# Kernel optimization log

Measured on AMD Instinct MI355X. Metric: run time of the kernel, lower is better.

## Reference

```python
import jax, jax.numpy as jnp
import numpy as np

NUM_NODES = 100000
NUM_EDGES = 3200000
D_IN, D_HID, D_OUT = 64, 64, 32


def setup_inputs() -> dict:
    key = jax.random.key(0)
    k1, k2, k3, k4, k5 = jax.random.split(key, 5)
    edge_index = jax.random.randint(k1, (2, NUM_EDGES), 0, NUM_NODES, dtype=jnp.int64)
    edge_weight = jax.random.uniform(k2, (NUM_EDGES,), dtype=jnp.float32)
    emb = jax.random.normal(k3, (NUM_NODES, D_IN), dtype=jnp.float32)
    # glorot-ish scaled weights for the two GCNConv layers
    W1 = jax.random.normal(k4, (D_IN, D_HID), dtype=jnp.float32) * (1.0 / np.sqrt(D_IN))
    b1 = jnp.zeros((D_HID,), dtype=jnp.float32)
    W2 = jax.random.normal(k5, (D_HID, D_OUT), dtype=jnp.float32) * (1.0 / np.sqrt(D_HID))
    b2 = jnp.zeros((D_OUT,), dtype=jnp.float32)
    return {"edge_index": edge_index, "edge_weight": edge_weight,
            "emb": emb, "W1": W1, "b1": b1, "W2": W2, "b2": b2}


def reference(edge_index, edge_weight, emb, W1, b1, W2, b2):
    N = emb.shape[0]
    row, col = edge_index[0], edge_index[1]
    # PyG gcn_norm: add self-loops (weight 1.0), symmetric normalization
    loop = jnp.arange(N, dtype=edge_index.dtype)
    row_f = jnp.concatenate([row, loop])
    col_f = jnp.concatenate([col, loop])
    ew_f = jnp.concatenate([edge_weight, jnp.ones((N,), dtype=edge_weight.dtype)])
    deg = jax.ops.segment_sum(ew_f, col_f, num_segments=N)          # [N]
    deg_inv_sqrt = jnp.where(deg > 0, jax.lax.rsqrt(deg), 0.0)      # inf -> 0
    norm = deg_inv_sqrt[row_f] * ew_f * deg_inv_sqrt[col_f]         # [E+N]

    def gcn_conv(x, W, b):
        x = x @ W                                                    # [N, d_out]
        msg = x[row_f] * norm[:, None]                               # [E+N, d_out]
        out = jax.ops.segment_sum(msg, col_f, num_segments=N)       # [N, d_out]
        return out + b

    x = jax.nn.relu(gcn_conv(emb, W1, b1))
    x = gcn_conv(x, W2, b2)
    # F.normalize(p=2, dim=1, eps=1e-12)
    l2 = jnp.linalg.norm(x, axis=1, keepdims=True)
    return x / jnp.maximum(l2, 1e-12)
```

## Files before the change

### kernel.cpp

```cpp
#include <hip/hip_runtime.h>
#include <hip/hip_fp16.h>
#include <math.h>

#define THREADS 256
#define BWIDTH 512
#define BSHIFT 9
#define CHUNK 3125

__global__ void init_kernel(const int* __restrict__ ei32, int* __restrict__ flag,
                            unsigned int* __restrict__ gcnt) {
    int t = threadIdx.x;
    gcnt[t] = 0u;
    if (t == 0) {
        int z = (ei32[1] == 0) + (ei32[3] == 0) + (ei32[5] == 0) + (ei32[7] == 0);
        *flag = (z == 4) ? 1 : 0;
    }
}

__device__ __forceinline__ int edge_at(const void* ei, int is64, size_t idx) {
    return is64 ? (int)((const long long*)ei)[idx] : ((const int*)ei)[idx];
}

__global__ void p1_count_kernel(const void* __restrict__ ei, const int* __restrict__ flag,
                                unsigned int* __restrict__ gcnt, unsigned int* __restrict__ table,
                                int E, int B) {
    __shared__ unsigned int lcnt[256];
    int t = threadIdx.x, b = blockIdx.x;
    lcnt[t] = 0u;
    __syncthreads();
    int is64 = *flag;
    int base = b * CHUNK;
    int end = min(E, base + CHUNK);
    for (int e = base + t; e < end; e += THREADS) {
        int c = edge_at(ei, is64, (size_t)E + e);
        atomicAdd(&lcnt[c >> BSHIFT], 1u);
    }
    __syncthreads();
    if (t < B) table[(size_t)b * 256 + t] = atomicAdd(&gcnt[t], lcnt[t]);
}

__global__ void p2_scan_kernel(const unsigned int* __restrict__ gcnt,
                               unsigned int* __restrict__ bstart, int B, int E) {
    int t = threadIdx.x;
    unsigned int v = (t < B) ? gcnt[t] : 0u;
    unsigned int incl = v;
    int lane = t & 63, wid = t >> 6;
#pragma unroll
    for (int off = 1; off < 64; off <<= 1) {
        unsigned int x = __shfl_up(incl, off);
        if (lane >= off) incl += x;
    }
    __shared__ unsigned int ws4[4];
    if (lane == 63) ws4[wid] = incl;
    __syncthreads();
    unsigned int wb = 0;
    for (int w = 0; w < wid; ++w) wb += ws4[w];
    unsigned int excl = wb + incl - v;
    if (t < B) bstart[t] = excl;
    if (t == 0) bstart[B] = (unsigned int)E;
}

__global__ void p3_scatter_kernel(const void* __restrict__ ei, const float* __restrict__ ew,
                                  const int* __restrict__ flag,
                                  const unsigned int* __restrict__ bstart,
                                  const unsigned int* __restrict__ table,
                                  int2* __restrict__ out, int E, int B) {
    __shared__ int2 stage[CHUNK];
    __shared__ unsigned char lbin[CHUNK];
    __shared__ unsigned short perm[CHUNK];
    __shared__ unsigned int lcnt[256];
    __shared__ unsigned int lcur[256];
    __shared__ int shiftb[256];
    __shared__ unsigned int ws4[4];

    int t = threadIdx.x, b = blockIdx.x;
    lcnt[t] = 0u;
    __syncthreads();
    int is64 = *flag;
    int base = b * CHUNK;
    int end = min(E, base + CHUNK);
    int n = end - base;
    for (int i = t; i < n; i += THREADS) {
        int e = base + i;
        int r = edge_at(ei, is64, (size_t)e);
        int c = edge_at(ei, is64, (size_t)E + e);
        int bin = c >> BSHIFT;
        stage[i] = make_int2(r | ((c & (BWIDTH - 1)) << 17), __float_as_int(ew[e]));
        lbin[i] = (unsigned char)bin;
        atomicAdd(&lcnt[bin], 1u);
    }
    __syncthreads();
    unsigned int v = lcnt[t];
    unsigned int incl = v;
    int lane = t & 63, wid = t >> 6;
#pragma unroll
    for (int off = 1; off < 64; off <<= 1) {
        unsigned int x = __shfl_up(incl, off);
        if (lane >= off) incl += x;
    }
    if (lane == 63) ws4[wid] = incl;
    __syncthreads();
    unsigned int wb = 0;
    for (int w = 0; w < wid; ++w) wb += ws4[w];
    unsigned int excl = wb + incl - v;
    lcur[t] = excl;
    shiftb[t] = (t < B) ? ((int)(bstart[t] + table[(size_t)b * 256 + t]) - (int)excl) : 0;
    __syncthreads();
    for (int i = t; i < n; i += THREADS) {
        unsigned int pos = atomicAdd(&lcur[lbin[i]], 1u);
        perm[pos] = (unsigned short)i;
    }
    __syncthreads();
    for (int k = t; k < n; k += THREADS) {
        int i = perm[k];
        int bin = lbin[i];
        out[(size_t)(shiftb[bin] + k)] = stage[i];
    }
}

__global__ void p5_bucket_kernel(const int2* __restrict__ bucketed,
                                 const unsigned int* __restrict__ bstart,
                                 float* __restrict__ dinv, int* __restrict__ colptr,
                                 int2* __restrict__ csr, int N, int E) {
    __shared__ unsigned int cnt[BWIDTH];
    __shared__ float deg[BWIDTH];
    __shared__ unsigned int cur[BWIDTH];
    __shared__ unsigned int ws4[4];

    int t = threadIdx.x, b = blockIdx.x;
    cnt[t] = 0u; cnt[t + 256] = 0u;
    deg[t] = 0.f; deg[t + 256] = 0.f;
    __syncthreads();
    unsigned int s = bstart[b], e2 = bstart[b + 1];
    for (unsigned int j = s + t; j < e2; j += THREADS) {
        int2 v = bucketed[j];
        unsigned int cl = ((unsigned int)v.x) >> 17;
        atomicAdd(&cnt[cl], 1u);
        atomicAdd(&deg[cl], __int_as_float(v.y));
    }
    __syncthreads();
    unsigned int a0 = cnt[2 * t], a1 = cnt[2 * t + 1];
    unsigned int sum = a0 + a1;
    unsigned int incl = sum;
    int lane = t & 63, wid = t >> 6;
#pragma unroll
    for (int off = 1; off < 64; off <<= 1) {
        unsigned int x = __shfl_up(incl, off);
        if (lane >= off) incl += x;
    }
    if (lane == 63) ws4[wid] = incl;
    __syncthreads();
    unsigned int wb = 0;
    for (int w = 0; w < wid; ++w) wb += ws4[w];
    unsigned int exclT = wb + incl - sum;
    unsigned int e0 = exclT, e1 = exclT + a0;
    int node0 = b << BSHIFT;
    int n0 = node0 + 2 * t, n1 = n0 + 1;
    float d0 = rsqrtf(deg[2 * t] + 1.0f);
    float d1 = rsqrtf(deg[2 * t + 1] + 1.0f);
    if (n0 < N) { colptr[n0] = (int)(s + e0); dinv[n0] = d0; }
    if (n1 < N) { colptr[n1] = (int)(s + e1); dinv[n1] = d1; }
    deg[2 * t] = d0;
    deg[2 * t + 1] = d1;
    cur[2 * t] = s + e0;
    cur[2 * t + 1] = s + e1;
    __syncthreads();
    for (unsigned int j = s + t; j < e2; j += THREADS) {
        int2 v = bucketed[j];
        unsigned int cl = ((unsigned int)v.x) >> 17;
        unsigned int pos = atomicAdd(&cur[cl], 1u);
        float w = __int_as_float(v.y) * deg[cl];
        csr[pos] = make_int2(v.x, __float_as_int(w));
    }
    if (b == 0 && t == 0) colptr[N] = E;
}

__device__ __forceinline__ float ldf(const float* p, size_t i) { return p[i]; }
__device__ __forceinline__ float ldf(const __half* p, size_t i) { return __half2float(p[i]); }

template <typename TIN, int DOUT>
__global__ void gemm_kernel(const TIN* __restrict__ X, const float* __restrict__ W,
                            const float* __restrict__ dinv, __half* __restrict__ Y, int N) {
    constexpr int RPB = 256 / DOUT;
    __shared__ float Wl[64 * DOUT];
    __shared__ float Xl[RPB * 64];
    int tid = threadIdx.x;
    for (int i = tid; i < 64 * DOUT; i += 256) Wl[i] = W[i];
    int base = blockIdx.x * RPB;
    for (int i = tid; i < RPB * 64; i += 256) {
        int rr = base + i / 64;
        Xl[i] = (rr < N) ? ldf(X, (size_t)rr * 64 + (i & 63)) : 0.f;
    }
    __syncthreads();
    int r = tid / DOUT, c = tid % DOUT;
    int row = base + r;
    if (row < N) {
        float acc = 0.f;
#pragma unroll
        for (int k = 0; k < 64; ++k) acc = fmaf(Xl[r * 64 + k], Wl[k * DOUT + c], acc);
        Y[(size_t)row * DOUT + c] = __float2half(acc * dinv[row]);
    }
}

__global__ void agg1_kernel(const __half* __restrict__ X1, const int* __restrict__ colptr,
                            const int2* __restrict__ csr, const float* __restrict__ dinv,
                            const float* __restrict__ bias, __half* __restrict__ H, int N) {
    int tid = threadIdx.x;
    int node = blockIdx.x * 4 + (tid >> 6);
    if (node >= N) return;
    int lane = tid & 63;
    int eo = lane >> 5;
    int dp = lane & 31;
    int s = colptr[node], e = colptr[node + 1];
    float acc0 = 0.f, acc1 = 0.f;
    int j = s;
    while (j + 16 <= e) {
        int2 vv[8];
#pragma unroll
        for (int k = 0; k < 8; ++k) vv[k] = csr[j + 2 * k + eo];
        __half2 hh[8];
#pragma unroll
        for (int k = 0; k < 8; ++k) {
            int r = vv[k].x & 0x1FFFF;
            hh[k] = *(const __half2*)(X1 + ((size_t)r << 6) + (dp << 1));
        }
#pragma unroll
        for (int k = 0; k < 8; ++k) {
            float2 x = __half22float2(hh[k]);
            float w = __int_as_float(vv[k].y);
            acc0 = fmaf(w, x.x, acc0);
            acc1 = fmaf(w, x.y, acc1);
        }
        j += 16;
    }
    for (; j < e; j += 2) {
        int jj = j + eo;
        float w = 0.f;
        int r = 0;
        if (jj < e) { int2 v = csr[jj]; r = v.x & 0x1FFFF; w = __int_as_float(v.y); }
        __half2 h = *(const __half2*)(X1 + ((size_t)r << 6) + (dp << 1));
        float2 x = __half22float2(h);
        acc0 = fmaf(w, x.x, acc0);
        acc1 = fmaf(w, x.y, acc1);
    }
    acc0 += __shfl_xor(acc0, 32);
    acc1 += __shfl_xor(acc1, 32);
    if (eo == 0) {
        float di = dinv[node];
        __half2 hs = *(const __half2*)(X1 + ((size_t)node << 6) + (dp << 1));
        float2 xs = __half22float2(hs);
        float a0 = fmaxf(bias[2 * dp + 0] + fmaf(di, xs.x, acc0), 0.f);
        float a1 = fmaxf(bias[2 * dp + 1] + fmaf(di, xs.y, acc1), 0.f);
        *(__half2*)(H + ((size_t)node << 6) + (dp << 1)) = __floats2half2_rn(a0, a1);
    }
}

__global__ void agg2_kernel(const __half* __restrict__ X2, const int* __restrict__ colptr,
                            const int2* __restrict__ csr, const float* __restrict__ dinv,
                            const float* __restrict__ bias, float* __restrict__ out, int N) {
    int tid = threadIdx.x;
    int node = blockIdx.x * 4 + (tid >> 6);
    if (node >= N) return;
    int lane = tid & 63;
    int eo = lane >> 4;
    int dp = lane & 15;
    int s = colptr[node], e = colptr[node + 1];
    float acc0 = 0.f, acc1 = 0.f;
    int j = s;
    while (j + 16 <= e) {
        int2 vv[4];
#pragma unroll
        for (int k = 0; k < 4; ++k) vv[k] = csr[j + 4 * k + eo];
        __half2 hh[4];
#pragma unroll
        for (int k = 0; k < 4; ++k) {
            int r = vv[k].x & 0x1FFFF;
            hh[k] = *(const __half2*)(X2 + ((size_t)r << 5) + (dp << 1));
        }
#pragma unroll
        for (int k = 0; k < 4; ++k) {
            float2 x = __half22float2(hh[k]);
            float w = __int_as_float(vv[k].y);
            acc0 = fmaf(w, x.x, acc0);
            acc1 = fmaf(w, x.y, acc1);
        }
        j += 16;
    }
    for (; j < e; j += 4) {
        int jj = j + eo;
        float w = 0.f;
        int r = 0;
        if (jj < e) { int2 v = csr[jj]; r = v.x & 0x1FFFF; w = __int_as_float(v.y); }
        __half2 h = *(const __half2*)(X2 + ((size_t)r << 5) + (dp << 1));
        float2 x = __half22float2(h);
        acc0 = fmaf(w, x.x, acc0);
        acc1 = fmaf(w, x.y, acc1);
    }
    acc0 += __shfl_xor(acc0, 16);
    acc1 += __shfl_xor(acc1, 16);
    acc0 += __shfl_xor(acc0, 32);
    acc1 += __shfl_xor(acc1, 32);
    float di = dinv[node];
    __half2 hs = *(const __half2*)(X2 + ((size_t)node << 5) + (dp << 1));
    float2 xs = __half22float2(hs);
    float a0 = bias[2 * dp + 0] + fmaf(di, xs.x, acc0);
    float a1 = bias[2 * dp + 1] + fmaf(di, xs.y, acc1);
    float ss = fmaf(a0, a0, a1 * a1);
#pragma unroll
    for (int m = 1; m <= 8; m <<= 1) ss += __shfl_xor(ss, m);
    float inv = 1.f / fmaxf(sqrtf(ss), 1e-12f);
    if (eo == 0) {
        *(float2*)(out + ((size_t)node << 5) + (dp << 1)) = make_float2(a0 * inv, a1 * inv);
    }
}

extern "C" void kernel_launch(void* const* d_in, const int* in_sizes, int n_in,
                              void* d_out, int out_size, void* d_ws, size_t ws_size,
                              hipStream_t stream) {
    const void* ei = d_in[0];
    const float* ew = (const float*)d_in[1];
    const float* emb = (const float*)d_in[2];
    const float* W1 = (const float*)d_in[3];
    const float* b1 = (const float*)d_in[4];
    const float* W2 = (const float*)d_in[5];
    const float* b2 = (const float*)d_in[6];
    float* outp = (float*)d_out;

    int E = in_sizes[0] / 2;
    int N = in_sizes[2] / 64;
    int B = (N + BWIDTH - 1) >> BSHIFT;
    int GP = (E + CHUNK - 1) / CHUNK;

    char* p = (char*)d_ws;
    auto alloc = [&](size_t bytes) {
        void* q = (void*)p;
        p += (bytes + 255) & ~(size_t)255;
        return q;
    };
    unsigned int* gcnt   = (unsigned int*)alloc(256 * 4);
    unsigned int* bstart = (unsigned int*)alloc(257 * 4);
    int*          flag   = (int*)alloc(256);
    unsigned int* table  = (unsigned int*)alloc((size_t)GP * 256 * 4);
    int2*   bucketed = (int2*)alloc((size_t)E * 8);
    int2*   csr      = (int2*)alloc(((size_t)E + 16) * 8);
    float*  dinv     = (float*)alloc((size_t)N * 4);
    int*    colptr   = (int*)alloc(((size_t)N + 1) * 4);
    __half* X1h      = (__half*)alloc((size_t)N * 64 * 2);
    __half* H        = (__half*)alloc((size_t)N * 64 * 2);
    __half* X2h      = X1h;

    init_kernel<<<1, 256, 0, stream>>>((const int*)ei, flag, gcnt);
    p1_count_kernel<<<GP, THREADS, 0, stream>>>(ei, flag, gcnt, table, E, B);
    p2_scan_kernel<<<1, 256, 0, stream>>>(gcnt, bstart, B, E);
    p3_scatter_kernel<<<GP, THREADS, 0, stream>>>(ei, ew, flag, bstart, table,
                                                  bucketed, E, B);
    p5_bucket_kernel<<<B, THREADS, 0, stream>>>(bucketed, bstart, dinv, colptr, csr, N, E);
    gemm_kernel<float, 64><<<(N + 3) / 4, THREADS, 0, stream>>>(emb, W1, dinv, X1h, N);
    agg1_kernel<<<(N + 3) / 4, THREADS, 0, stream>>>(X1h, colptr, csr, dinv, b1, H, N);
    gemm_kernel<__half, 32><<<(N + 7) / 8, THREADS, 0, stream>>>(H, W2, dinv, X2h, N);
    agg2_kernel<<<(N + 3) / 4, THREADS, 0, stream>>>(X2h, colptr, csr, dinv, b2, outp, N);
}
```

Before: 327.1 us.

## Pack CSR into 32-bit entries and aggregate feature slices in separate passes

Each CSR entry is packed into one 32-bit word holding a 17-bit source index and a 15-bit half-precision weight (sign bit dropped), halving edge-list traffic. Features are stored as 16-column slices so each aggregation pass gathers from a 3.2 MB table that fits in cache better. Aggregation runs as 4 passes for layer 1 and 2 passes for layer 2, plus a separate L2-normalize kernel. The cost is re-reading the CSR once per pass, extra launches, a temporary buffer, and lower precision on the edge weights.

```diff
diff --git a/kernel.cpp b/kernel.cpp
--- a/kernel.cpp
+++ b/kernel.cpp
@@ -19,6 +19,10 @@
 
 __device__ __forceinline__ int edge_at(const void* ei, int is64, size_t idx) {
     return is64 ? (int)((const long long*)ei)[idx] : ((const int*)ei)[idx];
+}
+
+__device__ __forceinline__ float wdec(unsigned int v) {
+    return __half2float(__ushort_as_half((unsigned short)(v & 0x7FFFu)));
 }
 
 __global__ void p1_count_kernel(const void* __restrict__ ei, const int* __restrict__ flag,
@@ -121,7 +125,7 @@
 __global__ void p5_bucket_kernel(const int2* __restrict__ bucketed,
                                  const unsigned int* __restrict__ bstart,
                                  float* __restrict__ dinv, int* __restrict__ colptr,
-                                 int2* __restrict__ csr, int N, int E) {
+                                 unsigned int* __restrict__ csrp, int N, int E) {
     __shared__ unsigned int cnt[BWIDTH];
     __shared__ float deg[BWIDTH];
     __shared__ unsigned int cur[BWIDTH];
@@ -170,148 +174,177 @@
         unsigned int cl = ((unsigned int)v.x) >> 17;
         unsigned int pos = atomicAdd(&cur[cl], 1u);
         float w = __int_as_float(v.y) * deg[cl];
-        csr[pos] = make_int2(v.x, __float_as_int(w));
+        unsigned short hb = __half_as_ushort(__float2half_rn(w));
+        csrp[pos] = (((unsigned int)v.x & 0x1FFFFu) << 15) | (unsigned int)(hb & 0x7FFFu);
     }
     if (b == 0 && t == 0) colptr[N] = E;
 }
 
-__device__ __forceinline__ float ldf(const float* p, size_t i) { return p[i]; }
-__device__ __forceinline__ float ldf(const __half* p, size_t i) { return __half2float(p[i]); }
-
-template <typename TIN, int DOUT>
-__global__ void gemm_kernel(const TIN* __restrict__ X, const float* __restrict__ W,
-                            const float* __restrict__ dinv, __half* __restrict__ Y, int N) {
-    constexpr int RPB = 256 / DOUT;
-    __shared__ float Wl[64 * DOUT];
-    __shared__ float Xl[RPB * 64];
+__global__ void gemm1_kernel(const float* __restrict__ X, const float* __restrict__ W,
+                             const float* __restrict__ dinv, __half* __restrict__ Y, int N) {
+    __shared__ float Wl[64 * 64];
+    __shared__ float Xl[4 * 64];
     int tid = threadIdx.x;
-    for (int i = tid; i < 64 * DOUT; i += 256) Wl[i] = W[i];
-    int base = blockIdx.x * RPB;
-    for (int i = tid; i < RPB * 64; i += 256) {
+    for (int i = tid; i < 64 * 64; i += 256) Wl[i] = W[i];
+    int base = blockIdx.x * 4;
+    for (int i = tid; i < 4 * 64; i += 256) {
         int rr = base + i / 64;
-        Xl[i] = (rr < N) ? ldf(X, (size_t)rr * 64 + (i & 63)) : 0.f;
-    }
-    __syncthreads();
-    int r = tid / DOUT, c = tid % DOUT;
+        Xl[i] = (rr < N) ? X[(size_t)rr * 64 + (i & 63)] : 0.f;
+    }
+    __syncthreads();
+    int r = tid >> 6, c = tid & 63;
     int row = base + r;
     if (row < N) {
         float acc = 0.f;
 #pragma unroll
-        for (int k = 0; k < 64; ++k) acc = fmaf(Xl[r * 64 + k], Wl[k * DOUT + c], acc);
-        Y[(size_t)row * DOUT + c] = __float2half(acc * dinv[row]);
-    }
-}
-
-__global__ void agg1_kernel(const __half* __restrict__ X1, const int* __restrict__ colptr,
-                            const int2* __restrict__ csr, const float* __restrict__ dinv,
-                            const float* __restrict__ bias, __half* __restrict__ H, int N) {
+        for (int k = 0; k < 64; ++k) acc = fmaf(Xl[r * 64 + k], Wl[k * 64 + c], acc);
+        Y[((size_t)(c >> 4) * N + row) * 16 + (c & 15)] = __float2half(acc * dinv[row]);
+    }
+}
+
+__global__ void gemm2_kernel(const __half* __restrict__ H, const float* __restrict__ W,
+                             const float* __restrict__ dinv, __half* __restrict__ Y, int N) {
+    __shared__ float Wl[64 * 32];
+    __shared__ float Xl[8 * 64];
+    int tid = threadIdx.x;
+    for (int i = tid; i < 64 * 32; i += 256) Wl[i] = W[i];
+    int base = blockIdx.x * 8;
+    for (int i = tid; i < 8 * 64; i += 256) {
+        int rr = base + i / 64;
+        int k = i & 63;
+        Xl[i] = (rr < N) ? __half2float(H[((size_t)(k >> 4) * N + rr) * 16 + (k & 15)]) : 0.f;
+    }
+    __syncthreads();
+    int r = tid >> 5, c = tid & 31;
+    int row = base + r;
+    if (row < N) {
+        float acc = 0.f;
+#pragma unroll
+        for (int k = 0; k < 64; ++k) acc = fmaf(Xl[r * 64 + k], Wl[k * 32 + c], acc);
+        Y[((size_t)(c >> 4) * N + row) * 16 + (c & 15)] = __float2half(acc * dinv[row]);
+    }
+}
+
+__global__ void agg1_pass_kernel(const __half* __restrict__ Xs, const int* __restrict__ colptr,
+                                 const unsigned int* __restrict__ csrp,
+                                 const float* __restrict__ dinv, const float* __restrict__ bias,
+                                 __half* __restrict__ Hs, int N) {
     int tid = threadIdx.x;
     int node = blockIdx.x * 4 + (tid >> 6);
     if (node >= N) return;
     int lane = tid & 63;
-    int eo = lane >> 5;
-    int dp = lane & 31;
+    int eo = lane >> 3;
+    int dp = lane & 7;
     int s = colptr[node], e = colptr[node + 1];
     float acc0 = 0.f, acc1 = 0.f;
     int j = s;
-    while (j + 16 <= e) {
-        int2 vv[8];
-#pragma unroll
-        for (int k = 0; k < 8; ++k) vv[k] = csr[j + 2 * k + eo];
-        __half2 hh[8];
-#pragma unroll
-        for (int k = 0; k < 8; ++k) {
-            int r = vv[k].x & 0x1FFFF;
-            hh[k] = *(const __half2*)(X1 + ((size_t)r << 6) + (dp << 1));
+    while (j + 32 <= e) {
+        unsigned int vv[4];
+#pragma unroll
+        for (int k = 0; k < 4; ++k) vv[k] = csrp[j + 8 * k + eo];
+        __half2 hh[4];
+#pragma unroll
+        for (int k = 0; k < 4; ++k) {
+            int r = (int)(vv[k] >> 15);
+            hh[k] = *(const __half2*)(Xs + ((size_t)r << 4) + (dp << 1));
         }
 #pragma unroll
-        for (int k = 0; k < 8; ++k) {
+        for (int k = 0; k < 4; ++k) {
             float2 x = __half22float2(hh[k]);
-            float w = __int_as_float(vv[k].y);
+            float w = wdec(vv[k]);
             acc0 = fmaf(w, x.x, acc0);
             acc1 = fmaf(w, x.y, acc1);
         }
-        j += 16;
-    }
-    for (; j < e; j += 2) {
+        j += 32;
+    }
+    for (; j < e; j += 8) {
         int jj = j + eo;
         float w = 0.f;
         int r = 0;
-        if (jj < e) { int2 v = csr[jj]; r = v.x & 0x1FFFF; w = __int_as_float(v.y); }
-        __half2 h = *(const __half2*)(X1 + ((size_t)r << 6) + (dp << 1));
+        if (jj < e) { unsigned int v = csrp[jj]; r = (int)(v >> 15); w = wdec(v); }
+        __half2 h = *(const __half2*)(Xs + ((size_t)r << 4) + (dp << 1));
         float2 x = __half22float2(h);
         acc0 = fmaf(w, x.x, acc0);
         acc1 = fmaf(w, x.y, acc1);
     }
-    acc0 += __shfl_xor(acc0, 32);
-    acc1 += __shfl_xor(acc1, 32);
+    acc0 += __shfl_xor(acc0, 8);  acc1 += __shfl_xor(acc1, 8);
+    acc0 += __shfl_xor(acc0, 16); acc1 += __shfl_xor(acc1, 16);
+    acc0 += __shfl_xor(acc0, 32); acc1 += __shfl_xor(acc1, 32);
     if (eo == 0) {
         float di = dinv[node];
-        __half2 hs = *(const __half2*)(X1 + ((size_t)node << 6) + (dp << 1));
+        __half2 hs = *(const __half2*)(Xs + ((size_t)node << 4) + (dp << 1));
         float2 xs = __half22float2(hs);
         float a0 = fmaxf(bias[2 * dp + 0] + fmaf(di, xs.x, acc0), 0.f);
         float a1 = fmaxf(bias[2 * dp + 1] + fmaf(di, xs.y, acc1), 0.f);
-        *(__half2*)(H + ((size_t)node << 6) + (dp << 1)) = __floats2half2_rn(a0, a1);
-    }
-}
-
-__global__ void agg2_kernel(const __half* __restrict__ X2, const int* __restrict__ colptr,
-                            const int2* __restrict__ csr, const float* __restrict__ dinv,
-                            const float* __restrict__ bias, float* __restrict__ out, int N) {
+        *(__half2*)(Hs + ((size_t)node << 4) + (dp << 1)) = __floats2half2_rn(a0, a1);
+    }
+}
+
+__global__ void agg2_pass_kernel(const __half* __restrict__ Xs, const int* __restrict__ colptr,
+                                 const unsigned int* __restrict__ csrp,
+                                 const float* __restrict__ dinv, const float* __restrict__ bias,
+                                 float* __restrict__ tempA, int ps, int N) {
     int tid = threadIdx.x;
     int node = blockIdx.x * 4 + (tid >> 6);
     if (node >= N) return;
     int lane = tid & 63;
-    int eo = lane >> 4;
-    int dp = lane & 15;
+    int eo = lane >> 3;
+    int dp = lane & 7;
     int s = colptr[node], e = colptr[node + 1];
     float acc0 = 0.f, acc1 = 0.f;
     int j = s;
-    while (j + 16 <= e) {
-        int2 vv[4];
-#pragma unroll
-        for (int k = 0; k < 4; ++k) vv[k] = csr[j + 4 * k + eo];
+    while (j + 32 <= e) {
+        unsigned int vv[4];
+#pragma unroll
+        for (int k = 0; k < 4; ++k) vv[k] = csrp[j + 8 * k + eo];
         __half2 hh[4];
 #pragma unroll
         for (int k = 0; k < 4; ++k) {
-            int r = vv[k].x & 0x1FFFF;
-            hh[k] = *(const __half2*)(X2 + ((size_t)r << 5) + (dp << 1));
+            int r = (int)(vv[k] >> 15);
+            hh[k] = *(const __half2*)(Xs + ((size_t)r << 4) + (dp << 1));
         }
 #pragma unroll
         for (int k = 0; k < 4; ++k) {
             float2 x = __half22float2(hh[k]);
-            float w = __int_as_float(vv[k].y);
+            float w = wdec(vv[k]);
             acc0 = fmaf(w, x.x, acc0);
             acc1 = fmaf(w, x.y, acc1);
         }
-        j += 16;
-    }
-    for (; j < e; j += 4) {
+        j += 32;
+    }
+    for (; j < e; j += 8) {
         int jj = j + eo;
         float w = 0.f;
         int r = 0;
-        if (jj < e) { int2 v = csr[jj]; r = v.x & 0x1FFFF; w = __int_as_float(v.y); }
-        __half2 h = *(const __half2*)(X2 + ((size_t)r << 5) + (dp << 1));
+        if (jj < e) { unsigned int v = csrp[jj]; r = (int)(v >> 15); w = wdec(v); }
+        __half2 h = *(const __half2*)(Xs + ((size_t)r << 4) + (dp << 1));
         float2 x = __half22float2(h);
         acc0 = fmaf(w, x.x, acc0);
         acc1 = fmaf(w, x.y, acc1);
     }
-    acc0 += __shfl_xor(acc0, 16);
-    acc1 += __shfl_xor(acc1, 16);
-    acc0 += __shfl_xor(acc0, 32);
-    acc1 += __shfl_xor(acc1, 32);
-    float di = dinv[node];
-    __half2 hs = *(const __half2*)(X2 + ((size_t)node << 5) + (dp << 1));
-    float2 xs = __half22float2(hs);
-    float a0 = bias[2 * dp + 0] + fmaf(di, xs.x, acc0);
-    float a1 = bias[2 * dp + 1] + fmaf(di, xs.y, acc1);
-    float ss = fmaf(a0, a0, a1 * a1);
-#pragma unroll
-    for (int m = 1; m <= 8; m <<= 1) ss += __shfl_xor(ss, m);
-    float inv = 1.f / fmaxf(sqrtf(ss), 1e-12f);
+    acc0 += __shfl_xor(acc0, 8);  acc1 += __shfl_xor(acc1, 8);
+    acc0 += __shfl_xor(acc0, 16); acc1 += __shfl_xor(acc1, 16);
+    acc0 += __shfl_xor(acc0, 32); acc1 += __shfl_xor(acc1, 32);
     if (eo == 0) {
-        *(float2*)(out + ((size_t)node << 5) + (dp << 1)) = make_float2(a0 * inv, a1 * inv);
-    }
+        float di = dinv[node];
+        __half2 hs = *(const __half2*)(Xs + ((size_t)node << 4) + (dp << 1));
+        float2 xs = __half22float2(hs);
+        float a0 = bias[2 * dp + 0] + fmaf(di, xs.x, acc0);
+        float a1 = bias[2 * dp + 1] + fmaf(di, xs.y, acc1);
+        *(float2*)(tempA + (size_t)node * 32 + ps * 16 + (dp << 1)) = make_float2(a0, a1);
+    }
+}
+
+__global__ void norm_kernel(const float* __restrict__ tempA, float* __restrict__ out, int N) {
+    int tid = threadIdx.x;
+    int node = blockIdx.x * 8 + (tid >> 5);
+    if (node >= N) return;
+    int d = tid & 31;
+    float a = tempA[(size_t)node * 32 + d];
+    float ss = a * a;
+#pragma unroll
+    for (int m = 1; m <= 16; m <<= 1) ss += __shfl_xor(ss, m);
+    out[(size_t)node * 32 + d] = a / fmaxf(sqrtf(ss), 1e-12f);
 }
 
 extern "C" void kernel_launch(void* const* d_in, const int* in_sizes, int n_in,
@@ -342,21 +375,30 @@
     int*          flag   = (int*)alloc(256);
     unsigned int* table  = (unsigned int*)alloc((size_t)GP * 256 * 4);
     int2*   bucketed = (int2*)alloc((size_t)E * 8);
-    int2*   csr      = (int2*)alloc(((size_t)E + 16) * 8);
+    unsigned int* csrp = (unsigned int*)alloc(((size_t)E + 64) * 4);
     float*  dinv     = (float*)alloc((size_t)N * 4);
     int*    colptr   = (int*)alloc(((size_t)N + 1) * 4);
     __half* X1h      = (__half*)alloc((size_t)N * 64 * 2);
     __half* H        = (__half*)alloc((size_t)N * 64 * 2);
     __half* X2h      = X1h;
+    float*  tempA    = (float*)alloc((size_t)N * 32 * 4);
 
     init_kernel<<<1, 256, 0, stream>>>((const int*)ei, flag, gcnt);
     p1_count_kernel<<<GP, THREADS, 0, stream>>>(ei, flag, gcnt, table, E, B);
     p2_scan_kernel<<<1, 256, 0, stream>>>(gcnt, bstart, B, E);
     p3_scatter_kernel<<<GP, THREADS, 0, stream>>>(ei, ew, flag, bstart, table,
                                                   bucketed, E, B);
-    p5_bucket_kernel<<<B, THREADS, 0, stream>>>(bucketed, bstart, dinv, colptr, csr, N, E);
-    gemm_kernel<float, 64><<<(N + 3) / 4, THREADS, 0, stream>>>(emb, W1, dinv, X1h, N);
-    agg1_kernel<<<(N + 3) / 4, THREADS, 0, stream>>>(X1h, colptr, csr, dinv, b1, H, N);
-    gemm_kernel<__half, 32><<<(N + 7) / 8, THREADS, 0, stream>>>(H, W2, dinv, X2h, N);
-    agg2_kernel<<<(N + 3) / 4, THREADS, 0, stream>>>(X2h, colptr, csr, dinv, b2, outp, N);
-}
+    p5_bucket_kernel<<<B, THREADS, 0, stream>>>(bucketed, bstart, dinv, colptr, csrp, N, E);
+    gemm1_kernel<<<(N + 3) / 4, THREADS, 0, stream>>>(emb, W1, dinv, X1h, N);
+    for (int s = 0; s < 4; ++s) {
+        agg1_pass_kernel<<<(N + 3) / 4, THREADS, 0, stream>>>(
+            X1h + (size_t)s * N * 16, colptr, csrp, dinv, b1 + 16 * s,
+            H + (size_t)s * N * 16, N);
+    }
+    gemm2_kernel<<<(N + 7) / 8, THREADS, 0, stream>>>(H, W2, dinv, X2h, N);
+    for (int s = 0; s < 2; ++s) {
+        agg2_pass_kernel<<<(N + 3) / 4, THREADS, 0, stream>>>(
+            X2h + (size_t)s * N * 16, colptr, csrp, dinv, b2 + 16 * s, tempA, s, N);
+    }
+    norm_kernel<<<(N + 7) / 8, THREADS, 0, stream>>>(tempA, outp, N);
+}
```

New measurement: 432.5 us. +32.2%, slower.

## Pack CSR entries into 32-bit words and use persistent GEMM kernels

Applied to the files above, without the earlier changes.

CSR entries shrink from an int2 (index plus float weight) to a single 32-bit word holding a 17-bit source index and a 15-bit fp16 weight with the sign bit dropped. Weights are nonnegative, so the sign bit is safe to drop. This halves edge-stream traffic in both aggregation passes. The aggregation loops are unrolled to 32 edges per step for more loads in flight, and the GEMMs become persistent grid-stride kernels that load W into shared memory once per block instead of once per four or eight rows. The trade-off is lower weight precision, and the index packing only works for N below 131072.

```diff
diff --git a/kernel.cpp b/kernel.cpp
--- a/kernel.cpp
+++ b/kernel.cpp
@@ -6,6 +6,8 @@
 #define BWIDTH 512
 #define BSHIFT 9
 #define CHUNK 3125
+#define G1ROWS 16
+#define G2ROWS 16
 
 __global__ void init_kernel(const int* __restrict__ ei32, int* __restrict__ flag,
                             unsigned int* __restrict__ gcnt) {
@@ -19,6 +21,10 @@
 
 __device__ __forceinline__ int edge_at(const void* ei, int is64, size_t idx) {
     return is64 ? (int)((const long long*)ei)[idx] : ((const int*)ei)[idx];
+}
+
+__device__ __forceinline__ float wdec(unsigned int v) {
+    return __half2float(__ushort_as_half((unsigned short)(v & 0x7FFFu)));
 }
 
 __global__ void p1_count_kernel(const void* __restrict__ ei, const int* __restrict__ flag,
@@ -121,7 +127,7 @@
 __global__ void p5_bucket_kernel(const int2* __restrict__ bucketed,
                                  const unsigned int* __restrict__ bstart,
                                  float* __restrict__ dinv, int* __restrict__ colptr,
-                                 int2* __restrict__ csr, int N, int E) {
+                                 unsigned int* __restrict__ csrp, int N, int E) {
     __shared__ unsigned int cnt[BWIDTH];
     __shared__ float deg[BWIDTH];
     __shared__ unsigned int cur[BWIDTH];
@@ -170,41 +176,82 @@
         unsigned int cl = ((unsigned int)v.x) >> 17;
         unsigned int pos = atomicAdd(&cur[cl], 1u);
         float w = __int_as_float(v.y) * deg[cl];
-        csr[pos] = make_int2(v.x, __float_as_int(w));
+        unsigned short hb = __half_as_ushort(__float2half_rn(w));
+        csrp[pos] = (((unsigned int)v.x & 0x1FFFFu) << 15) | (unsigned int)(hb & 0x7FFFu);
     }
     if (b == 0 && t == 0) colptr[N] = E;
 }
 
-__device__ __forceinline__ float ldf(const float* p, size_t i) { return p[i]; }
-__device__ __forceinline__ float ldf(const __half* p, size_t i) { return __half2float(p[i]); }
-
-template <typename TIN, int DOUT>
-__global__ void gemm_kernel(const TIN* __restrict__ X, const float* __restrict__ W,
-                            const float* __restrict__ dinv, __half* __restrict__ Y, int N) {
-    constexpr int RPB = 256 / DOUT;
-    __shared__ float Wl[64 * DOUT];
-    __shared__ float Xl[RPB * 64];
+__global__ void gemm1_kernel(const float* __restrict__ X, const float* __restrict__ W,
+                             const float* __restrict__ dinv, __half* __restrict__ Y,
+                             int N, int tiles) {
+    __shared__ float Wl[64 * 64];
+    __shared__ float Xl[G1ROWS * 64];
     int tid = threadIdx.x;
-    for (int i = tid; i < 64 * DOUT; i += 256) Wl[i] = W[i];
-    int base = blockIdx.x * RPB;
-    for (int i = tid; i < RPB * 64; i += 256) {
-        int rr = base + i / 64;
-        Xl[i] = (rr < N) ? ldf(X, (size_t)rr * 64 + (i & 63)) : 0.f;
-    }
-    __syncthreads();
-    int r = tid / DOUT, c = tid % DOUT;
-    int row = base + r;
-    if (row < N) {
-        float acc = 0.f;
-#pragma unroll
-        for (int k = 0; k < 64; ++k) acc = fmaf(Xl[r * 64 + k], Wl[k * DOUT + c], acc);
-        Y[(size_t)row * DOUT + c] = __float2half(acc * dinv[row]);
+    for (int i = tid; i < 64 * 64; i += 256) Wl[i] = W[i];
+    int wid = tid >> 6, c = tid & 63;
+    __syncthreads();
+    for (int tile = blockIdx.x; tile < tiles; tile += gridDim.x) {
+        int base = tile * G1ROWS;
+        for (int i = tid; i < G1ROWS * 64; i += 256) {
+            int rr = base + (i >> 6);
+            Xl[i] = (rr < N) ? X[(size_t)rr * 64 + (i & 63)] : 0.f;
+        }
+        __syncthreads();
+#pragma unroll
+        for (int rg = 0; rg < G1ROWS / 4; ++rg) {
+            int r = rg * 4 + wid;
+            int row = base + r;
+            if (row < N) {
+                float acc = 0.f;
+#pragma unroll
+                for (int k = 0; k < 64; ++k) acc = fmaf(Xl[r * 64 + k], Wl[k * 64 + c], acc);
+                Y[(size_t)row * 64 + c] = __float2half(acc * dinv[row]);
+            }
+        }
+        __syncthreads();
+    }
+}
+
+__global__ void gemm2_kernel(const __half* __restrict__ H, const float* __restrict__ W,
+                             const float* __restrict__ dinv, __half* __restrict__ Y,
+                             int N, int tiles) {
+    __shared__ float Wl[64 * 32];
+    __shared__ float Xl[G2ROWS * 64];
+    int tid = threadIdx.x;
+    for (int i = tid; i < 64 * 32; i += 256) Wl[i] = W[i];
+    int rg0 = tid >> 5, c = tid & 31;
+    __syncthreads();
+    for (int tile = blockIdx.x; tile < tiles; tile += gridDim.x) {
+        int base = tile * G2ROWS;
+        for (int i = tid; i < G2ROWS * 32; i += 256) {
+            int rr = base + (i >> 5);
+            int kk = (i & 31) << 1;
+            float2 f = make_float2(0.f, 0.f);
+            if (rr < N) f = __half22float2(*(const __half2*)(H + (size_t)rr * 64 + kk));
+            Xl[(i >> 5) * 64 + kk] = f.x;
+            Xl[(i >> 5) * 64 + kk + 1] = f.y;
+        }
+        __syncthreads();
+#pragma unroll
+        for (int rg = 0; rg < G2ROWS / 8; ++rg) {
+            int r = rg * 8 + rg0;
+            int row = base + r;
+            if (row < N) {
+                float acc = 0.f;
+#pragma unroll
+                for (int k = 0; k < 64; ++k) acc = fmaf(Xl[r * 64 + k], Wl[k * 32 + c], acc);
+                Y[(size_t)row * 32 + c] = __float2half(acc * dinv[row]);
+            }
+        }
+        __syncthreads();
     }
 }
 
 __global__ void agg1_kernel(const __half* __restrict__ X1, const int* __restrict__ colptr,
-                            const int2* __restrict__ csr, const float* __restrict__ dinv,
-                            const float* __restrict__ bias, __half* __restrict__ H, int N) {
+                            const unsigned int* __restrict__ csrp,
+                            const float* __restrict__ dinv, const float* __restrict__ bias,
+                            __half* __restrict__ H, int N) {
     int tid = threadIdx.x;
     int node = blockIdx.x * 4 + (tid >> 6);
     if (node >= N) return;
@@ -214,30 +261,30 @@
     int s = colptr[node], e = colptr[node + 1];
     float acc0 = 0.f, acc1 = 0.f;
     int j = s;
-    while (j + 16 <= e) {
-        int2 vv[8];
-#pragma unroll
-        for (int k = 0; k < 8; ++k) vv[k] = csr[j + 2 * k + eo];
-        __half2 hh[8];
-#pragma unroll
-        for (int k = 0; k < 8; ++k) {
-            int r = vv[k].x & 0x1FFFF;
+    while (j + 32 <= e) {
+        unsigned int vv[16];
+#pragma unroll
+        for (int k = 0; k < 16; ++k) vv[k] = csrp[j + 2 * k + eo];
+        __half2 hh[16];
+#pragma unroll
+        for (int k = 0; k < 16; ++k) {
+            int r = (int)(vv[k] >> 15);
             hh[k] = *(const __half2*)(X1 + ((size_t)r << 6) + (dp << 1));
         }
 #pragma unroll
-        for (int k = 0; k < 8; ++k) {
+        for (int k = 0; k < 16; ++k) {
             float2 x = __half22float2(hh[k]);
-            float w = __int_as_float(vv[k].y);
+            float w = wdec(vv[k]);
             acc0 = fmaf(w, x.x, acc0);
             acc1 = fmaf(w, x.y, acc1);
         }
-        j += 16;
+        j += 32;
     }
     for (; j < e; j += 2) {
         int jj = j + eo;
         float w = 0.f;
         int r = 0;
-        if (jj < e) { int2 v = csr[jj]; r = v.x & 0x1FFFF; w = __int_as_float(v.y); }
+        if (jj < e) { unsigned int v = csrp[jj]; r = (int)(v >> 15); w = wdec(v); }
         __half2 h = *(const __half2*)(X1 + ((size_t)r << 6) + (dp << 1));
         float2 x = __half22float2(h);
         acc0 = fmaf(w, x.x, acc0);
@@ -256,8 +303,9 @@
 }
 
 __global__ void agg2_kernel(const __half* __restrict__ X2, const int* __restrict__ colptr,
-                            const int2* __restrict__ csr, const float* __restrict__ dinv,
-                            const float* __restrict__ bias, float* __restrict__ out, int N) {
+                            const unsigned int* __restrict__ csrp,
+                            const float* __restrict__ dinv, const float* __restrict__ bias,
+                            float* __restrict__ out, int N) {
     int tid = threadIdx.x;
     int node = blockIdx.x * 4 + (tid >> 6);
     if (node >= N) return;
@@ -267,30 +315,30 @@
     int s = colptr[node], e = colptr[node + 1];
     float acc0 = 0.f, acc1 = 0.f;
     int j = s;
-    while (j + 16 <= e) {
-        int2 vv[4];
-#pragma unroll
-        for (int k = 0; k < 4; ++k) vv[k] = csr[j + 4 * k + eo];
-        __half2 hh[4];
-#pragma unroll
-        for (int k = 0; k < 4; ++k) {
-            int r = vv[k].x & 0x1FFFF;
+    while (j + 32 <= e) {
+        unsigned int vv[8];
+#pragma unroll
+        for (int k = 0; k < 8; ++k) vv[k] = csrp[j + 4 * k + eo];
+        __half2 hh[8];
+#pragma unroll
+        for (int k = 0; k < 8; ++k) {
+            int r = (int)(vv[k] >> 15);
             hh[k] = *(const __half2*)(X2 + ((size_t)r << 5) + (dp << 1));
         }
 #pragma unroll
-        for (int k = 0; k < 4; ++k) {
+        for (int k = 0; k < 8; ++k) {
             float2 x = __half22float2(hh[k]);
-            float w = __int_as_float(vv[k].y);
+            float w = wdec(vv[k]);
             acc0 = fmaf(w, x.x, acc0);
             acc1 = fmaf(w, x.y, acc1);
         }
-        j += 16;
+        j += 32;
     }
     for (; j < e; j += 4) {
         int jj = j + eo;
         float w = 0.f;
         int r = 0;
-        if (jj < e) { int2 v = csr[jj]; r = v.x & 0x1FFFF; w = __int_as_float(v.y); }
+        if (jj < e) { unsigned int v = csrp[jj]; r = (int)(v >> 15); w = wdec(v); }
         __half2 h = *(const __half2*)(X2 + ((size_t)r << 5) + (dp << 1));
         float2 x = __half22float2(h);
         acc0 = fmaf(w, x.x, acc0);
@@ -342,21 +390,24 @@
     int*          flag   = (int*)alloc(256);
     unsigned int* table  = (unsigned int*)alloc((size_t)GP * 256 * 4);
     int2*   bucketed = (int2*)alloc((size_t)E * 8);
-    int2*   csr      = (int2*)alloc(((size_t)E + 16) * 8);
+    unsigned int* csrp = (unsigned int*)alloc(((size_t)E + 64) * 4);
     float*  dinv     = (float*)alloc((size_t)N * 4);
     int*    colptr   = (int*)alloc(((size_t)N + 1) * 4);
     __half* X1h      = (__half*)alloc((size_t)N * 64 * 2);
     __half* H        = (__half*)alloc((size_t)N * 64 * 2);
     __half* X2h      = X1h;
 
+    int tiles1 = (N + G1ROWS - 1) / G1ROWS;
+    int tiles2 = (N + G2ROWS - 1) / G2ROWS;
+
     init_kernel<<<1, 256, 0, stream>>>((const int*)ei, flag, gcnt);
     p1_count_kernel<<<GP, THREADS, 0, stream>>>(ei, flag, gcnt, table, E, B);
     p2_scan_kernel<<<1, 256, 0, stream>>>(gcnt, bstart, B, E);
     p3_scatter_kernel<<<GP, THREADS, 0, stream>>>(ei, ew, flag, bstart, table,
                                                   bucketed, E, B);
-    p5_bucket_kernel<<<B, THREADS, 0, stream>>>(bucketed, bstart, dinv, colptr, csr, N, E);
-    gemm_kernel<float, 64><<<(N + 3) / 4, THREADS, 0, stream>>>(emb, W1, dinv, X1h, N);
-    agg1_kernel<<<(N + 3) / 4, THREADS, 0, stream>>>(X1h, colptr, csr, dinv, b1, H, N);
-    gemm_kernel<__half, 32><<<(N + 7) / 8, THREADS, 0, stream>>>(H, W2, dinv, X2h, N);
-    agg2_kernel<<<(N + 3) / 4, THREADS, 0, stream>>>(X2h, colptr, csr, dinv, b2, outp, N);
-}
+    p5_bucket_kernel<<<B, THREADS, 0, stream>>>(bucketed, bstart, dinv, colptr, csrp, N, E);
+    gemm1_kernel<<<1024, THREADS, 0, stream>>>(emb, W1, dinv, X1h, N, tiles1);
+    agg1_kernel<<<(N + 3) / 4, THREADS, 0, stream>>>(X1h, colptr, csrp, dinv, b1, H, N);
+    gemm2_kernel<<<1024, THREADS, 0, stream>>>(H, W2, dinv, X2h, N, tiles2);
+    agg2_kernel<<<(N + 3) / 4, THREADS, 0, stream>>>(X2h, colptr, csrp, dinv, b2, outp, N);
+}
```

New measurement: 346.2 us. 5.8% more time.
